# Performance work log

Hardware: AMD Instinct MI355X
Metric: run time of the kernel (lower is better)

The kernel has to match this reference:

```python
import jax, jax.numpy as jnp
import numpy as np

TEMPERATURE = 8.0  # sqrt(d_head=64)
CLAMP = 15.0
EPS = 1e-6


def setup_inputs() -> dict:
    key = jax.random.key(0)
    kq, kk, kv, km = jax.random.split(key, 4)
    B, Lq, Lk, D = 16, 2048, 2048, 64
    q = jax.random.normal(kq, (B, Lq, D), dtype=jnp.float32)
    k = jax.random.normal(kk, (B, Lk, D), dtype=jnp.float32)
    v = jax.random.normal(kv, (B, Lk, D), dtype=jnp.float32)
    mask = jax.random.randint(km, (B, Lq, Lk), 0, 2).astype(jnp.float32)
    return {"q": q, "k": k, "v": v, "mask": mask}


def masked_softmax(x, m, axis=-1):
    # clamp -> multiply by mask -> stable exp -> multiply by mask -> normalize
    x = jnp.clip(x, -CLAMP, CLAMP)
    x = x * m
    e_x = jnp.exp(x - jnp.max(x, axis=axis, keepdims=True))
    e_x = e_x * m
    return e_x / (jnp.sum(e_x, axis=axis, keepdims=True) + EPS)


def reference(q, k, v, mask):
    # scores: [B, Lq, Lk]
    attn = jnp.einsum('bqd,bkd->bqk', q, k) / TEMPERATURE
    attn = masked_softmax(attn, mask, axis=2)
    # dropout is identity in eval mode (deterministic reference)
    output = jnp.einsum('bqk,bkd->bqd', attn, v)
    return (output, attn)
```

## Files before the change

kernel.cpp:

```cpp
#include <hip/hip_runtime.h>
#include <stdint.h>

#define NB 16
#define LQ 2048
#define LK 2048
#define DH 64
#define QT 16
#define NW 16
#define STRIP (NW * 16)
#define NIT (LK / STRIP)

typedef short bf16x8 __attribute__((ext_vector_type(8)));
typedef float f32x4 __attribute__((ext_vector_type(4)));

__device__ __forceinline__ unsigned short f2bf(float f) {
    union { float f; uint32_t u; } v; v.f = f;
    uint32_t u = v.u;
    u += 0x7FFFu + ((u >> 16) & 1u);
    return (unsigned short)(u >> 16);
}
__device__ __forceinline__ float bf2f(unsigned short h) {
    union { uint32_t u; float f; } v; v.u = ((uint32_t)h) << 16;
    return v.f;
}
__device__ __forceinline__ uint32_t pack2(float lo, float hi) {
    return (uint32_t)f2bf(lo) | ((uint32_t)f2bf(hi) << 16);
}

__global__ void convert_kernel(const float* __restrict__ q, const float* __restrict__ k,
                               const float* __restrict__ v,
                               unsigned short* __restrict__ qb,
                               unsigned short* __restrict__ kb,
                               unsigned short* __restrict__ vtb) {
    int bid = blockIdx.x;
    int tid = threadIdx.x;
    if (bid < 2048) {
        const float* src = (bid < 1024) ? q : k;
        unsigned short* dst = (bid < 1024) ? qb : kb;
        int64_t off = (int64_t)(bid & 1023) * 2048 + (int64_t)tid * 8;
        float4 a = *(const float4*)(src + off);
        float4 b4 = *(const float4*)(src + off + 4);
        uint4 o;
        o.x = pack2(a.x, a.y);
        o.y = pack2(a.z, a.w);
        o.z = pack2(b4.x, b4.y);
        o.w = pack2(b4.z, b4.w);
        *(uint4*)(dst + off) = o;
    } else {
        __shared__ unsigned short tile[64][72];
        int bid2 = bid - 2048;
        int bb = bid2 >> 5, kt = bid2 & 31;
        int k0 = kt * 64;
        int krow = tid >> 2, dc = (tid & 3) * 16;
        const float* vp = v + ((int64_t)(bb * LK) + k0 + krow) * DH + dc;
        float4 x0 = *(const float4*)(vp);
        float4 x1 = *(const float4*)(vp + 4);
        float4 x2 = *(const float4*)(vp + 8);
        float4 x3 = *(const float4*)(vp + 12);
        float vals[16] = {x0.x, x0.y, x0.z, x0.w, x1.x, x1.y, x1.z, x1.w,
                          x2.x, x2.y, x2.z, x2.w, x3.x, x3.y, x3.z, x3.w};
        #pragma unroll
        for (int i = 0; i < 16; ++i) tile[dc + i][krow] = f2bf(vals[i]);
        __syncthreads();
        int d = tid >> 2, kc = (tid & 3) * 16;
        uint4 r0 = *(const uint4*)&tile[d][kc];
        uint4 r1 = *(const uint4*)&tile[d][kc + 8];
        unsigned short* op = vtb + ((int64_t)(bb * DH) + d) * LK + k0 + kc;
        *(uint4*)op = r0;
        *(uint4*)(op + 8) = r1;
    }
}

__launch_bounds__(1024, 8)
__global__ void attn_kernel(const unsigned short* __restrict__ qb,
                            const unsigned short* __restrict__ kb,
                            const unsigned short* __restrict__ vtb,
                            const float* __restrict__ mask,
                            float* __restrict__ out, float* __restrict__ attn) {
    extern __shared__ char smem[];
    float* denom_part = (float*)(smem + QT * LK * 2);
    float* denF       = (float*)(smem + QT * LK * 2 + 1024);
    float* pp         = (float*)(smem + QT * LK * 2 + 1088);

    int bid = blockIdx.x;
    int swz = (bid & 7) * 256 + (bid >> 3);
    int b = swz >> 7;
    int q0 = (swz & 127) * QT;

    int tid = threadIdx.x;
    int lane = tid & 63;
    int wave = tid >> 6;
    int lr = lane & 15, lg = lane >> 4;

    bf16x8 qf0, qf1;
    {
        const unsigned short* qp = qb + ((int64_t)(b * LQ + q0 + lr)) * DH + 8 * lg;
        qf0 = *(const bf16x8*)qp;
        qf1 = *(const bf16x8*)(qp + 32);
    }

    float dsum = 0.f;

    {
        const unsigned short* kpw =
            kb + (int64_t)b * LK * DH + (wave * 16 + lr) * DH + 8 * lg;
        const float* mrow =
            mask + ((int64_t)(b * LQ + q0 + lr)) * LK + wave * 16 + lg * 4;
        bf16x8 kf0 = *(const bf16x8*)kpw;
        bf16x8 kf1 = *(const bf16x8*)(kpw + 32);
        float4 mcur = *(const float4*)mrow;
        float4 mn1  = *(const float4*)(mrow + STRIP);
        #pragma unroll
        for (int kt = 0; kt < NIT; ++kt) {
            float4 mn2;
            if (kt + 2 < NIT) mn2 = *(const float4*)(mrow + (kt + 2) * STRIP);
            bf16x8 nk0, nk1;
            if (kt + 1 < NIT) {
                const unsigned short* np = kpw + (int64_t)(kt + 1) * STRIP * DH;
                nk0 = *(const bf16x8*)np;
                nk1 = *(const bf16x8*)(np + 32);
            }
            f32x4 acc = {0.f, 0.f, 0.f, 0.f};
            acc = __builtin_amdgcn_mfma_f32_16x16x32_bf16(kf0, qf0, acc, 0, 0, 0);
            acc = __builtin_amdgcn_mfma_f32_16x16x32_bf16(kf1, qf1, acc, 0, 0, 0);
            float mv[4] = {mcur.x, mcur.y, mcur.z, mcur.w};
            unsigned short eb[4];
            #pragma unroll
            for (int j = 0; j < 4; ++j) {
                float s = acc[j] * 0.125f;
                s = fminf(fmaxf(s, -15.0f), 15.0f);
                unsigned short p = f2bf(__expf(s));
                eb[j] = (mv[j] != 0.f) ? p : (unsigned short)0;
                dsum += bf2f(eb[j]);
            }
            uint2 u;
            u.x = (uint32_t)eb[0] | ((uint32_t)eb[1] << 16);
            u.y = (uint32_t)eb[2] | ((uint32_t)eb[3] << 16);
            int c = kt * STRIP + wave * 16 + lg * 4;
            int byteoff = (lr * 4096 + c * 2) ^ ((lr & 7) << 4);
            *(uint2*)(smem + byteoff) = u;
            kf0 = nk0; kf1 = nk1;
            mcur = mn1; mn1 = mn2;
        }
    }

    dsum += __shfl_xor(dsum, 16);
    dsum += __shfl_xor(dsum, 32);
    if (lane < 16) denom_part[wave * 16 + lane] = dsum;
    __syncthreads();

    {
        int r = wave;
        float den = 1e-6f;
        #pragma unroll
        for (int w = 0; w < NW; ++w) den += denom_part[w * 16 + r];
        if (lane == 0) denF[r] = den;
        float inv = 1.0f / den;
        float* ap = attn + ((int64_t)(b * LQ + q0 + r)) * LK;
        int rowbase = r * 4096;
        int sw = (r & 7) << 4;
        int c0l = lane * 8;
        #pragma unroll
        for (int i = 0; i < 4; ++i) {
            int byteoff = (rowbase + (i * 512 + c0l) * 2) ^ sw;
            bf16x8 ev = *(const bf16x8*)(smem + byteoff);
            f32x4 o0, o1;
            o0[0] = bf2f((unsigned short)ev[0]) * inv;
            o0[1] = bf2f((unsigned short)ev[1]) * inv;
            o0[2] = bf2f((unsigned short)ev[2]) * inv;
            o0[3] = bf2f((unsigned short)ev[3]) * inv;
            o1[0] = bf2f((unsigned short)ev[4]) * inv;
            o1[1] = bf2f((unsigned short)ev[5]) * inv;
            o1[2] = bf2f((unsigned short)ev[6]) * inv;
            o1[3] = bf2f((unsigned short)ev[7]) * inv;
            __builtin_nontemporal_store(o0, (f32x4*)(ap + i * 512 + c0l));
            __builtin_nontemporal_store(o1, (f32x4*)(ap + i * 512 + c0l + 4));
        }
    }

    f32x4 pacc = {0.f, 0.f, 0.f, 0.f};
    int cw = (wave & 3) * 16, kq = wave >> 2;
    {
        const unsigned short* vp =
            vtb + ((int64_t)(b * DH + cw + lr)) * LK + kq * 512 + 8 * lg;
        int rowbase = lr * 4096;
        int sw = (lr & 7) << 4;
        int kk0 = kq * 512;
        #pragma unroll 4
        for (int kk = 0; kk < 512; kk += 32) {
            int byteoff = (rowbase + (kk0 + kk + 8 * lg) * 2) ^ sw;
            bf16x8 ef = *(const bf16x8*)(smem + byteoff);
            bf16x8 vf = *(const bf16x8*)(vp + kk);
            pacc = __builtin_amdgcn_mfma_f32_16x16x32_bf16(ef, vf, pacc, 0, 0, 0);
        }
    }
    if (kq != 0) {
        #pragma unroll
        for (int j = 0; j < 4; ++j)
            pp[((kq - 1) * 4 + (wave & 3)) * 256 + (lg * 4 + j) * 16 + lr] = pacc[j];
    }
    __syncthreads();
    if (kq == 0) {
        int c4 = wave & 3;
        #pragma unroll
        for (int j = 0; j < 4; ++j) {
            int r = lg * 4 + j;
            float den = denF[r];
            float val = pacc[j] + pp[(c4) * 256 + r * 16 + lr] +
                        pp[(4 + c4) * 256 + r * 16 + lr] +
                        pp[(8 + c4) * 256 + r * 16 + lr];
            out[((int64_t)(b * LQ + q0 + r)) * DH + cw + lr] = val / den;
        }
    }
}

extern "C" void kernel_launch(void* const* d_in, const int* in_sizes, int n_in,
                              void* d_out, int out_size, void* d_ws, size_t ws_size,
                              hipStream_t stream) {
    const float* q    = (const float*)d_in[0];
    const float* k    = (const float*)d_in[1];
    const float* v    = (const float*)d_in[2];
    const float* mask = (const float*)d_in[3];
    float* out  = (float*)d_out;
    float* attn = out + (int64_t)NB * LQ * DH;

    unsigned short* qb  = (unsigned short*)d_ws;
    unsigned short* kb  = qb + (int64_t)NB * LQ * DH;
    unsigned short* vtb = kb + (int64_t)NB * LK * DH;

    (void)hipFuncSetAttribute((const void*)attn_kernel,
                              hipFuncAttributeMaxDynamicSharedMemorySize, 78912);

    convert_kernel<<<2560, 256, 0, stream>>>(q, k, v, qb, kb, vtb);
    attn_kernel<<<2048, 1024, 78912, stream>>>(qb, kb, vtb, mask, out, attn);
}
```

Before: 227.9 us.

## Persistent blocks process eight query tiles with double-buffered score staging

Result: slower. 233.4 us (+2.4%).

```diff
diff --git a/kernel.cpp b/kernel.cpp
--- a/kernel.cpp
+++ b/kernel.cpp
@@ -7,8 +7,9 @@
 #define DH 64
 #define QT 16
 #define NW 16
-#define STRIP (NW * 16)
-#define NIT (LK / STRIP)
+#define STRIP 256
+#define NIT 8
+#define TPB 8
 
 typedef short bf16x8 __attribute__((ext_vector_type(8)));
 typedef float f32x4 __attribute__((ext_vector_type(4)));
@@ -71,49 +72,36 @@
     }
 }
 
-__launch_bounds__(1024, 8)
+__launch_bounds__(1024, 4)
 __global__ void attn_kernel(const unsigned short* __restrict__ qb,
                             const unsigned short* __restrict__ kb,
                             const unsigned short* __restrict__ vtb,
                             const float* __restrict__ mask,
                             float* __restrict__ out, float* __restrict__ attn) {
     extern __shared__ char smem[];
-    float* denom_part = (float*)(smem + QT * LK * 2);
-    float* denF       = (float*)(smem + QT * LK * 2 + 1024);
-    float* pp         = (float*)(smem + QT * LK * 2 + 1088);
+    float* denb = (float*)(smem + 131072);
+    float* pp   = (float*)(smem + 131072 + 128);
 
     int bid = blockIdx.x;
-    int swz = (bid & 7) * 256 + (bid >> 3);
-    int b = swz >> 7;
-    int q0 = (swz & 127) * QT;
+    int b  = (bid & 7) * 2 + (bid >> 7);
+    int qc = (bid >> 3) & 15;
 
     int tid = threadIdx.x;
-    int lane = tid & 63;
-    int wave = tid >> 6;
+    int lane = tid & 63, wave = tid >> 6;
     int lr = lane & 15, lg = lane >> 4;
 
-    bf16x8 qf0, qf1;
-    {
-        const unsigned short* qp = qb + ((int64_t)(b * LQ + q0 + lr)) * DH + 8 * lg;
-        qf0 = *(const bf16x8*)qp;
-        qf1 = *(const bf16x8*)(qp + 32);
-    }
-
-    float dsum = 0.f;
-
-    {
-        const unsigned short* kpw =
-            kb + (int64_t)b * LK * DH + (wave * 16 + lr) * DH + 8 * lg;
-        const float* mrow =
-            mask + ((int64_t)(b * LQ + q0 + lr)) * LK + wave * 16 + lg * 4;
+    const int64_t brow = (int64_t)b * LQ;
+    const unsigned short* kpw =
+        kb + (int64_t)b * LK * DH + (wave * 16 + lr) * DH + 8 * lg;
+
+    auto ph1 = [&](int q0, char* ebuf) {
+        const unsigned short* qp = qb + (brow + q0 + lr) * DH + 8 * lg;
+        bf16x8 qf0 = *(const bf16x8*)qp;
+        bf16x8 qf1 = *(const bf16x8*)(qp + 32);
         bf16x8 kf0 = *(const bf16x8*)kpw;
         bf16x8 kf1 = *(const bf16x8*)(kpw + 32);
-        float4 mcur = *(const float4*)mrow;
-        float4 mn1  = *(const float4*)(mrow + STRIP);
         #pragma unroll
         for (int kt = 0; kt < NIT; ++kt) {
-            float4 mn2;
-            if (kt + 2 < NIT) mn2 = *(const float4*)(mrow + (kt + 2) * STRIP);
             bf16x8 nk0, nk1;
             if (kt + 1 < NIT) {
                 const unsigned short* np = kpw + (int64_t)(kt + 1) * STRIP * DH;
@@ -123,47 +111,76 @@
             f32x4 acc = {0.f, 0.f, 0.f, 0.f};
             acc = __builtin_amdgcn_mfma_f32_16x16x32_bf16(kf0, qf0, acc, 0, 0, 0);
             acc = __builtin_amdgcn_mfma_f32_16x16x32_bf16(kf1, qf1, acc, 0, 0, 0);
-            float mv[4] = {mcur.x, mcur.y, mcur.z, mcur.w};
             unsigned short eb[4];
             #pragma unroll
             for (int j = 0; j < 4; ++j) {
-                float s = acc[j] * 0.125f;
-                s = fminf(fmaxf(s, -15.0f), 15.0f);
-                unsigned short p = f2bf(__expf(s));
-                eb[j] = (mv[j] != 0.f) ? p : (unsigned short)0;
-                dsum += bf2f(eb[j]);
+                float sc = acc[j] * 0.125f;
+                sc = fminf(fmaxf(sc, -15.0f), 15.0f);
+                eb[j] = f2bf(__expf(sc));
             }
             uint2 u;
             u.x = (uint32_t)eb[0] | ((uint32_t)eb[1] << 16);
             u.y = (uint32_t)eb[2] | ((uint32_t)eb[3] << 16);
             int c = kt * STRIP + wave * 16 + lg * 4;
             int byteoff = (lr * 4096 + c * 2) ^ ((lr & 7) << 4);
-            *(uint2*)(smem + byteoff) = u;
+            *(uint2*)(ebuf + byteoff) = u;
             kf0 = nk0; kf1 = nk1;
-            mcur = mn1; mn1 = mn2;
-        }
-    }
-
-    dsum += __shfl_xor(dsum, 16);
-    dsum += __shfl_xor(dsum, 32);
-    if (lane < 16) denom_part[wave * 16 + lane] = dsum;
-    __syncthreads();
-
-    {
+        }
+    };
+
+    f32x4 mk[8];
+
+    auto mload = [&](int q0) {
+        const float* mrow = mask + (brow + q0 + wave) * LK;
+        int c0l = lane * 8;
+        #pragma unroll
+        for (int i = 0; i < 4; ++i) {
+            mk[2 * i]     = *(const f32x4*)(mrow + i * 512 + c0l);
+            mk[2 * i + 1] = *(const f32x4*)(mrow + i * 512 + c0l + 4);
+        }
+    };
+    auto mconsume = [&](char* ebuf, int par) {
         int r = wave;
-        float den = 1e-6f;
-        #pragma unroll
-        for (int w = 0; w < NW; ++w) den += denom_part[w * 16 + r];
-        if (lane == 0) denF[r] = den;
-        float inv = 1.0f / den;
-        float* ap = attn + ((int64_t)(b * LQ + q0 + r)) * LK;
-        int rowbase = r * 4096;
-        int sw = (r & 7) << 4;
+        int rowbase = r * 4096, sw = (r & 7) << 4;
         int c0l = lane * 8;
+        float dsum = 0.f;
         #pragma unroll
         for (int i = 0; i < 4; ++i) {
             int byteoff = (rowbase + (i * 512 + c0l) * 2) ^ sw;
-            bf16x8 ev = *(const bf16x8*)(smem + byteoff);
+            bf16x8 pv = *(const bf16x8*)(ebuf + byteoff);
+            uint32_t packed[4];
+            #pragma unroll
+            for (int h = 0; h < 4; ++h) {
+                float m0 = (h < 2) ? mk[2 * i][2 * h] : mk[2 * i + 1][2 * h - 4];
+                float m1 = (h < 2) ? mk[2 * i][2 * h + 1] : mk[2 * i + 1][2 * h - 3];
+                unsigned short e0 = (m0 != 0.f) ? (unsigned short)pv[2 * h] : (unsigned short)0;
+                unsigned short e1 = (m1 != 0.f) ? (unsigned short)pv[2 * h + 1] : (unsigned short)0;
+                dsum += bf2f(e0) + bf2f(e1);
+                packed[h] = (uint32_t)e0 | ((uint32_t)e1 << 16);
+            }
+            uint4 wb = {packed[0], packed[1], packed[2], packed[3]};
+            int byteoff2 = (rowbase + (i * 512 + c0l) * 2) ^ sw;
+            *(uint4*)(ebuf + byteoff2) = wb;
+        }
+        dsum += __shfl_xor(dsum, 1);
+        dsum += __shfl_xor(dsum, 2);
+        dsum += __shfl_xor(dsum, 4);
+        dsum += __shfl_xor(dsum, 8);
+        dsum += __shfl_xor(dsum, 16);
+        dsum += __shfl_xor(dsum, 32);
+        if (lane == 0) denb[par * 16 + r] = dsum + 1e-6f;
+    };
+
+    auto atw = [&](int q0, char* ebuf, int par) {
+        int r = wave;
+        float inv = 1.0f / denb[par * 16 + r];
+        float* ap = attn + (brow + q0 + r) * LK;
+        int rowbase = r * 4096, sw = (r & 7) << 4;
+        int c0l = lane * 8;
+        #pragma unroll
+        for (int i = 0; i < 4; ++i) {
+            int byteoff = (rowbase + (i * 512 + c0l) * 2) ^ sw;
+            bf16x8 ev = *(const bf16x8*)(ebuf + byteoff);
             f32x4 o0, o1;
             o0[0] = bf2f((unsigned short)ev[0]) * inv;
             o0[1] = bf2f((unsigned short)ev[1]) * inv;
@@ -173,44 +190,71 @@
             o1[1] = bf2f((unsigned short)ev[5]) * inv;
             o1[2] = bf2f((unsigned short)ev[6]) * inv;
             o1[3] = bf2f((unsigned short)ev[7]) * inv;
-            __builtin_nontemporal_store(o0, (f32x4*)(ap + i * 512 + c0l));
-            __builtin_nontemporal_store(o1, (f32x4*)(ap + i * 512 + c0l + 4));
-        }
+            *(f32x4*)(ap + i * 512 + c0l) = o0;
+            *(f32x4*)(ap + i * 512 + c0l + 4) = o1;
+        }
+    };
+
+    char* eb0 = smem;
+    char* eb1 = smem + 65536;
+
+    {
+        int q0 = (qc * TPB) * QT;
+        ph1(q0, eb0);
+        __syncthreads();
+        mload(q0);
+        mconsume(eb0, 0);
+        __syncthreads();
     }
 
-    f32x4 pacc = {0.f, 0.f, 0.f, 0.f};
-    int cw = (wave & 3) * 16, kq = wave >> 2;
-    {
-        const unsigned short* vp =
-            vtb + ((int64_t)(b * DH + cw + lr)) * LK + kq * 512 + 8 * lg;
-        int rowbase = lr * 4096;
-        int sw = (lr & 7) << 4;
-        int kk0 = kq * 512;
-        #pragma unroll 4
-        for (int kk = 0; kk < 512; kk += 32) {
-            int byteoff = (rowbase + (kk0 + kk + 8 * lg) * 2) ^ sw;
-            bf16x8 ef = *(const bf16x8*)(smem + byteoff);
-            bf16x8 vf = *(const bf16x8*)(vp + kk);
-            pacc = __builtin_amdgcn_mfma_f32_16x16x32_bf16(ef, vf, pacc, 0, 0, 0);
-        }
-    }
-    if (kq != 0) {
-        #pragma unroll
-        for (int j = 0; j < 4; ++j)
-            pp[((kq - 1) * 4 + (wave & 3)) * 256 + (lg * 4 + j) * 16 + lr] = pacc[j];
-    }
-    __syncthreads();
-    if (kq == 0) {
-        int c4 = wave & 3;
-        #pragma unroll
-        for (int j = 0; j < 4; ++j) {
-            int r = lg * 4 + j;
-            float den = denF[r];
-            float val = pacc[j] + pp[(c4) * 256 + r * 16 + lr] +
-                        pp[(4 + c4) * 256 + r * 16 + lr] +
-                        pp[(8 + c4) * 256 + r * 16 + lr];
-            out[((int64_t)(b * LQ + q0 + r)) * DH + cw + lr] = val / den;
-        }
+    for (int i = 0; i < TPB; ++i) {
+        int par = i & 1;
+        char* ebuf = par ? eb1 : eb0;
+        char* nbuf = par ? eb0 : eb1;
+        int q0  = (qc * TPB + i) * QT;
+        int q0n = (qc * TPB + i + 1) * QT;
+
+        f32x4 pacc = {0.f, 0.f, 0.f, 0.f};
+        int cw = (wave & 3) * 16, kq = wave >> 2;
+        {
+            const unsigned short* vp =
+                vtb + ((int64_t)(b * DH + cw + lr)) * LK + kq * 512 + 8 * lg;
+            int rowbase = lr * 4096;
+            int sw = (lr & 7) << 4;
+            int kk0 = kq * 512;
+            #pragma unroll 4
+            for (int kk = 0; kk < 512; kk += 32) {
+                int byteoff = (rowbase + (kk0 + kk + 8 * lg) * 2) ^ sw;
+                bf16x8 ef = *(const bf16x8*)(ebuf + byteoff);
+                bf16x8 vf = *(const bf16x8*)(vp + kk);
+                pacc = __builtin_amdgcn_mfma_f32_16x16x32_bf16(ef, vf, pacc, 0, 0, 0);
+            }
+        }
+        if (kq != 0) {
+            #pragma unroll
+            for (int j = 0; j < 4; ++j)
+                pp[((kq - 1) * 4 + (wave & 3)) * 256 + (lg * 4 + j) * 16 + lr] = pacc[j];
+        }
+        __syncthreads();
+        if (kq == 0) {
+            int c4 = wave & 3;
+            #pragma unroll
+            for (int j = 0; j < 4; ++j) {
+                int r = lg * 4 + j;
+                float dd = denb[par * 16 + r];
+                float val = pacc[j] + pp[(c4) * 256 + r * 16 + lr] +
+                            pp[(4 + c4) * 256 + r * 16 + lr] +
+                            pp[(8 + c4) * 256 + r * 16 + lr];
+                out[(brow + q0 + r) * DH + cw + lr] = val / dd;
+            }
+        }
+        if (i + 1 < TPB) ph1(q0n, nbuf);
+        __syncthreads();
+
+        if (i + 1 < TPB) mload(q0n);
+        atw(q0, ebuf, par);
+        if (i + 1 < TPB) mconsume(nbuf, par ^ 1);
+        __syncthreads();
     }
 }
 
@@ -229,8 +273,8 @@
     unsigned short* vtb = kb + (int64_t)NB * LK * DH;
 
     (void)hipFuncSetAttribute((const void*)attn_kernel,
-                              hipFuncAttributeMaxDynamicSharedMemorySize, 78912);
+                              hipFuncAttributeMaxDynamicSharedMemorySize, 143488);
 
     convert_kernel<<<2560, 256, 0, stream>>>(q, k, v, qb, kb, vtb);
-    attn_kernel<<<2048, 1024, 78912, stream>>>(qb, kb, vtb, mask, out, attn);
-}
+    attn_kernel<<<256, 1024, 143488, stream>>>(qb, kb, vtb, mask, out, attn);
+}
```
